# Kernel tuning notes

Measured on AMD Instinct MI355X. Metric: run time of the kernel, lower is better.

## Reference

```python
import jax, jax.numpy as jnp
import numpy as np

N = 100_000      # nodes
E = 1_600_000    # edges (avg degree 16)
IN_DIM = 165
HIDDEN = 64
OUT_DIM = 2


def setup_inputs() -> dict:
    key = jax.random.key(0)
    ks = jax.random.split(key, 10)
    x = jax.random.normal(ks[0], (N, IN_DIM), dtype=jnp.float32)
    edge_index = jax.random.randint(ks[1], (2, E), 0, N, dtype=jnp.int32)
    def lin(k, fan_in, fan_out):
        lim = 1.0 / np.sqrt(fan_in)
        return jax.random.uniform(k, (fan_in, fan_out), jnp.float32, -lim, lim)
    # SAGEConv: lin_l (neighbor path, with bias), lin_r (root path, no bias)
    W1l = lin(ks[2], IN_DIM, HIDDEN); b1 = jnp.zeros((HIDDEN,), jnp.float32)
    W1r = lin(ks[3], IN_DIM, HIDDEN)
    W2l = lin(ks[4], HIDDEN, HIDDEN); b2 = jnp.zeros((HIDDEN,), jnp.float32)
    W2r = lin(ks[5], HIDDEN, HIDDEN)
    Wc = lin(ks[6], HIDDEN, OUT_DIM)
    bc = jax.random.uniform(ks[7], (OUT_DIM,), jnp.float32, -0.1, 0.1)
    return {"x": x, "edge_index": edge_index, "W1l": W1l, "b1": b1, "W1r": W1r,
            "W2l": W2l, "b2": b2, "W2r": W2r, "Wc": Wc, "bc": bc}


def _sage_conv(h, src, dst, Wl, bl, Wr):
    # mean-aggregate source features at destination nodes, then two linears
    msg = h[src]                                              # [E, D] gather
    agg = jax.ops.segment_sum(msg, dst, num_segments=N)       # [N, D] scatter-add
    cnt = jax.ops.segment_sum(jnp.ones((src.shape[0], 1), h.dtype), dst,
                              num_segments=N)                 # [N, 1] in-degree
    mean = agg / jnp.maximum(cnt, 1.0)
    return mean @ Wl + bl + h @ Wr


def reference(x, edge_index, W1l, b1, W1r, W2l, b2, W2r, Wc, bc):
    src, dst = edge_index[0], edge_index[1]
    h = jax.nn.relu(_sage_conv(x, src, dst, W1l, b1, W1r))
    # dropout is a no-op at inference (training=False)
    h = jax.nn.relu(_sage_conv(h, src, dst, W2l, b2, W2r))
    return h @ Wc + bc
```

## Files before the change

kernel.cpp:

```cpp
#include <hip/hip_runtime.h>
#include <hip/hip_fp16.h>
#include <cstdint>

#define NN 100000
#define NE 1600000
#define INDIM 165
#define HID 64
#define KP1 192
#define KP2 64

constexpr int BSH = 7;
constexpr int BNODES = 128;
constexpr int NBUK = (NN + BNODES - 1) / BNODES;
constexpr int SC_CHUNK = 8192;
constexpr int BCAP = 2816;

typedef _Float16 f16x8 __attribute__((ext_vector_type(8)));
typedef _Float16 h2 __attribute__((ext_vector_type(2)));
typedef float f32x4 __attribute__((ext_vector_type(4)));


__global__ __launch_bounds__(256) void k_bscan(const int* __restrict__ bcnt,
                                               int* __restrict__ bbase) {
    __shared__ int wsum[4];
    const int tid = threadIdx.x, lane = tid & 63, wid = tid >> 6;
    int v[4];
    int tsum = 0;
#pragma unroll
    for (int i = 0; i < 4; ++i) {
        int idx = tid * 4 + i;
        v[i] = (idx < NBUK) ? bcnt[idx] : 0;
        tsum += v[i];
    }
    int x = tsum;
#pragma unroll
    for (int off = 1; off < 64; off <<= 1) {
        int y = __shfl_up(x, off, 64);
        if (lane >= off) x += y;
    }
    if (lane == 63) wsum[wid] = x;
    __syncthreads();
    int woff = 0;
#pragma unroll
    for (int w = 0; w < 4; ++w)
        if (w < wid) woff += wsum[w];
    int run = woff + x - tsum;
#pragma unroll
    for (int i = 0; i < 4; ++i) {
        int idx = tid * 4 + i;
        if (idx < NBUK) bbase[idx] = run;
        run += v[i];
    }
    if (tid == 255) bbase[NBUK] = woff + x;
}


__global__ __launch_bounds__(256) void k_scatter(const int* __restrict__ src,
                                                 const int* __restrict__ dst,
                                                 int* __restrict__ bcnt,
                                                 unsigned* __restrict__ Eb, int ne) {
    __shared__ int hist[NBUK];
    __shared__ int base[NBUK];
    const int tid = threadIdx.x;
    const int cs = blockIdx.x * SC_CHUNK;
    for (int b = tid; b < NBUK; b += 256) hist[b] = 0;
    __syncthreads();
    unsigned pack[SC_CHUNK / 256];
#pragma unroll 8
    for (int i = 0; i < SC_CHUNK / 256; ++i) {
        int e = cs + i * 256 + tid;
        if (e < ne) {
            int b = dst[e] >> BSH;
            int r = atomicAdd(&hist[b], 1);
            pack[i] = (unsigned)((b << 13) | r);
        } else {
            pack[i] = 0xFFFFFFFFu;
        }
    }
    __syncthreads();
    for (int b = tid; b < NBUK; b += 256) {
        int c = hist[b];
        base[b] = c ? atomicAdd(&bcnt[b], c) : 0;
    }
    __syncthreads();
#pragma unroll 8
    for (int i = 0; i < SC_CHUNK / 256; ++i) {
        if (pack[i] != 0xFFFFFFFFu) {
            int e = cs + i * 256 + tid;
            int b = pack[i] >> 13, r = pack[i] & 8191;
            int pos = base[b] + r;
            if (pos < BCAP)
                Eb[(size_t)b * BCAP + pos] =
                    (unsigned)src[e] | ((unsigned)(dst[e] & (BNODES - 1)) << 17);
        }
    }
}


__global__ __launch_bounds__(256) void k_csrb(const unsigned* __restrict__ Eb,
                                              const int* __restrict__ bbase,
                                              int* __restrict__ rowptr,
                                              int* __restrict__ col, int n) {
    __shared__ int cnt[BNODES];
    __shared__ int pref[BNODES];
    const int tid = threadIdx.x;
    const int gb = bbase[blockIdx.x];
    const int m = bbase[blockIdx.x + 1] - gb;
    const unsigned* eb = Eb + (size_t)blockIdx.x * BCAP;
    for (int i = tid; i < BNODES; i += 256) cnt[i] = 0;
    __syncthreads();
    for (int e = tid; e < m; e += 256)
        atomicAdd(&cnt[eb[e] >> 17], 1);
    __syncthreads();
    if (tid < 64) {
        int c0 = cnt[tid * 2], c1 = cnt[tid * 2 + 1];
        int s = c0 + c1;
        int x = s;
#pragma unroll
        for (int off = 1; off < 64; off <<= 1) {
            int y = __shfl_up(x, off, 64);
            if (tid >= off) x += y;
        }
        int ex = x - s;
        pref[tid * 2] = ex;
        pref[tid * 2 + 1] = ex + c0;
    }
    __syncthreads();
    const int nodeBase = blockIdx.x * BNODES;
    for (int i = tid; i < BNODES; i += 256) {
        int gn = nodeBase + i;
        if (gn < n) rowptr[gn] = gb + pref[i];
        cnt[i] = 0;
    }
    __syncthreads();
    for (int e = tid; e < m; e += 256) {
        unsigned v = eb[e];
        int d = (int)(v >> 17);
        int r = atomicAdd(&cnt[d], 1);
        col[gb + pref[d] + r] = (int)(v & 0x1FFFFu);
    }
    if (blockIdx.x == 0 && tid == 0) rowptr[n] = bbase[NBUK];
}


__global__ __launch_bounds__(256) void k_cvt(const float* __restrict__ X,
                                             const float* __restrict__ W1l,
                                             const float* __restrict__ W1r,
                                             const float* __restrict__ W2l,
                                             const float* __restrict__ W2r,
                                             _Float16* __restrict__ Xh,
                                             _Float16* __restrict__ Wt1,
                                             _Float16* __restrict__ Wt2) {
    constexpr int XB = (NN * 24) / 256;
    if (blockIdx.x < XB) {
        int g = blockIdx.x * 256 + threadIdx.x;
        int row = g / 24;
        int col0 = (g - row * 24) * 8;
        f16x8 h;
#pragma unroll
        for (int i = 0; i < 8; ++i) {
            int c = col0 + i;
            h[i] = (_Float16)((c < INDIM) ? X[(size_t)row * INDIM + c] : 0.f);
        }
        *(f16x8*)&Xh[(size_t)row * KP1 + col0] = h;
    } else {
        int o = (blockIdx.x - XB) * 256 + threadIdx.x;
        if (o < 128 * KP1) {
            int c = o / KP1, k = o - c * KP1;
            float v = 0.f;
            if (k < INDIM) v = (c < HID) ? W1l[k * HID + c] : W1r[k * HID + (c - HID)];
            Wt1[o] = (_Float16)v;
        } else {
            int p = o - 128 * KP1;
            int c = p / KP2, k = p - c * KP2;
            float v = (c < HID) ? W2l[k * HID + c] : W2r[k * HID + (c - HID)];
            Wt2[p] = (_Float16)v;
        }
    }
}


template <int KPAD>
__global__ __launch_bounds__(256, 4) void k_linear(const _Float16* __restrict__ Xh,
                                                   const _Float16* __restrict__ Wt,
                                                   _Float16* __restrict__ Y,
                                                   _Float16* __restrict__ Rh, int n) {
    const int tid = threadIdx.x;
    const int lane = tid & 63;
    const int w = tid >> 6;
    const int jn = lane & 15;
    const int kq = lane >> 4;
    const int gn0 = blockIdx.x * 64 + w * 16 + jn;
    const int gn = (gn0 < n) ? gn0 : (n - 1);

    const _Float16* xp = Xh + (size_t)gn * KPAD + kq * 8;
    const _Float16* wp = Wt + (size_t)jn * KPAD + kq * 8;

    f16x8 xf[KPAD / 32];
#pragma unroll
    for (int c = 0; c < KPAD / 32; ++c)
        xf[c] = *(const f16x8*)(xp + c * 32);

    f32x4 acc[8];
#pragma unroll
    for (int t = 0; t < 8; ++t) acc[t] = (f32x4){0.f, 0.f, 0.f, 0.f};

#pragma unroll
    for (int c = 0; c < KPAD / 32; ++c) {
#pragma unroll
        for (int t = 0; t < 8; ++t) {
            const f16x8 wa = *(const f16x8*)(wp + t * (16 * KPAD) + c * 32);
            acc[t] = __builtin_amdgcn_mfma_f32_16x16x32_f16(wa, xf[c], acc[t], 0, 0, 0);
        }
    }

    if (gn0 < n) {
#pragma unroll
        for (int t = 0; t < 8; ++t) {
            const int cb = (t & 3) * 16 + kq * 4;
            union { _Float16 h[4]; uint2 u; } u;
#pragma unroll
            for (int r = 0; r < 4; ++r) u.h[r] = (_Float16)acc[t][r];
            _Float16* dstp = (t < 4) ? (Y + (size_t)gn * HID + cb)
                                     : (Rh + (size_t)gn * HID + cb);
            *(uint2*)dstp = u.u;
        }
    }
}


__device__ __forceinline__ void acc2(float& ax, float& ay, h2 v) {
    ax += (float)v[0];
    ay += (float)v[1];
}

template <bool CLS>
__global__ __launch_bounds__(256) void k_agg(const _Float16* __restrict__ Y,
                                             const _Float16* __restrict__ Rm,
                                             const float* __restrict__ bias,
                                             const int* __restrict__ rowptr,
                                             const int* __restrict__ col,
                                             _Float16* __restrict__ H,
                                             const float* __restrict__ Wc,
                                             const float* __restrict__ bc,
                                             float* __restrict__ out, int n) {
    const int lane = threadIdx.x & 63;
    const int node = blockIdx.x * 4 + (threadIdx.x >> 6);
    if (node >= n) return;
    const int half_ = lane >> 5;
    const unsigned fp = (unsigned)(lane & 31);
    const h2* __restrict__ Y2 = (const h2*)Y;
    const int s = rowptr[node], e = rowptr[node + 1];
    float ax0 = 0.f, ay0 = 0.f, ax1 = 0.f, ay1 = 0.f;
    int i = s + half_;
    for (; i + 14 < e; i += 16) {
        int c[8];
#pragma unroll
        for (int j = 0; j < 8; ++j) c[j] = col[i + 2 * j];
        h2 y[8];
#pragma unroll
        for (int j = 0; j < 8; ++j) y[j] = Y2[(unsigned)c[j] * 32u + fp];
#pragma unroll
        for (int j = 0; j < 8; j += 2) {
            acc2(ax0, ay0, y[j]);
            acc2(ax1, ay1, y[j + 1]);
        }
    }
    for (; i + 6 < e; i += 8) {
        int c[4];
#pragma unroll
        for (int j = 0; j < 4; ++j) c[j] = col[i + 2 * j];
        h2 y[4];
#pragma unroll
        for (int j = 0; j < 4; ++j) y[j] = Y2[(unsigned)c[j] * 32u + fp];
        acc2(ax0, ay0, y[0]);
        acc2(ax1, ay1, y[1]);
        acc2(ax0, ay0, y[2]);
        acc2(ax1, ay1, y[3]);
    }
    for (; i < e; i += 2)
        acc2(ax0, ay0, Y2[(unsigned)col[i] * 32u + fp]);
    float ax = ax0 + ax1, ay = ay0 + ay1;
    ax += __shfl_xor(ax, 32, 64);
    ay += __shfl_xor(ay, 32, 64);
    const float vx = __shfl(ax, lane >> 1, 64);
    const float vy = __shfl(ay, lane >> 1, 64);
    const float acc = (lane & 1) ? vy : vx;
    const int deg = e - s;
    float h = acc / (float)(deg > 1 ? deg : 1) + bias[lane] +
              (float)Rm[(size_t)node * HID + lane];
    h = fmaxf(h, 0.f);
    if (!CLS) {
        H[(size_t)node * HID + lane] = (_Float16)h;
    } else {
        float p0 = h * Wc[lane * 2 + 0];
        float p1 = h * Wc[lane * 2 + 1];
#pragma unroll
        for (int off = 32; off > 0; off >>= 1) {
            p0 += __shfl_xor(p0, off, 64);
            p1 += __shfl_xor(p1, off, 64);
        }
        if (lane == 0) {
            out[(size_t)node * 2 + 0] = p0 + bc[0];
            out[(size_t)node * 2 + 1] = p1 + bc[1];
        }
    }
}


extern "C" void kernel_launch(void* const* d_in, const int* in_sizes, int n_in,
                              void* d_out, int out_size, void* d_ws, size_t ws_size,
                              hipStream_t stream) {
    const float* x   = (const float*)d_in[0];
    const int*   ei  = (const int*)d_in[1];
    const float* W1l = (const float*)d_in[2];
    const float* b1  = (const float*)d_in[3];
    const float* W1r = (const float*)d_in[4];
    const float* W2l = (const float*)d_in[5];
    const float* b2  = (const float*)d_in[6];
    const float* W2r = (const float*)d_in[7];
    const float* Wc  = (const float*)d_in[8];
    const float* bc  = (const float*)d_in[9];
    float* out = (float*)d_out;
    const int* src = ei;
    const int* dst = ei + NE;

    char* base = (char*)d_ws;
    size_t off = 0;
    auto alloc = [&](size_t bytes) {
        void* p = base + off;
        off = (off + bytes + 255) & ~(size_t)255;
        return p;
    };
    int*      bcnt    = (int*)alloc((size_t)NBUK * 4);
    int*      bbase   = (int*)alloc((size_t)(NBUK + 1) * 4);
    int*      rowptr  = (int*)alloc((size_t)(NN + 1) * 4);
    int*      col     = (int*)alloc((size_t)NE * 4);
    _Float16* Y       = (_Float16*)alloc((size_t)NN * HID * 2 + 256);
    _Float16* Rh      = (_Float16*)alloc((size_t)NN * HID * 2);
    _Float16* Hh      = (_Float16*)alloc((size_t)NN * HID * 2);
    _Float16* Xh      = (_Float16*)alloc((size_t)NN * KP1 * 2);
    _Float16* Wt1     = (_Float16*)alloc((size_t)128 * KP1 * 2);
    _Float16* Wt2     = (_Float16*)alloc((size_t)128 * KP2 * 2);
    unsigned* Eb      = (unsigned*)Y;

    const int sb = (NE + SC_CHUNK - 1) / SC_CHUNK;
    constexpr int XB = (NN * 24) / 256;
    const int cvb = XB + (128 * KP1 + 128 * KP2 + 255) / 256;

    hipMemsetAsync(bcnt, 0, (size_t)NBUK * 4, stream);
    k_scatter<<<sb, 256, 0, stream>>>(src, dst, bcnt, Eb, NE);
    k_bscan<<<1, 256, 0, stream>>>(bcnt, bbase);
    k_csrb<<<NBUK, 256, 0, stream>>>(Eb, bbase, rowptr, col, NN);

    k_cvt<<<cvb, 256, 0, stream>>>(x, W1l, W1r, W2l, W2r, Xh, Wt1, Wt2);

    k_linear<KP1><<<(NN + 63) / 64, 256, 0, stream>>>(Xh, Wt1, Y, Rh, NN);
    k_agg<false><<<(NN + 3) / 4, 256, 0, stream>>>(Y, Rh, b1, rowptr, col, Hh,
                                                   nullptr, nullptr, nullptr, NN);
    k_linear<KP2><<<(NN + 63) / 64, 256, 0, stream>>>(Hh, Wt2, Y, Rh, NN);
    k_agg<true><<<(NN + 3) / 4, 256, 0, stream>>>(Y, Rh, b2, rowptr, col, nullptr,
                                                  Wc, bc, out, NN);
}
```

Measured before the change: 360.4 us.

## Fuse fp32-to-fp16 input conversion into first linear; widen aggregation gathers to 8 bytes

The first-layer linear kernel now reads the fp32 input features directly and converts them to fp16 in registers, so the separate conversion pass and the padded fp16 copy of X are gone. This drops one full write and read of a roughly 38 MB intermediate. The mean-aggregation kernel now splits each wave into four edge lanes that each gather 4 halves (8 bytes) per load instead of two lanes gathering 2 halves, followed by a wider shuffle reduction. The fused linear makes unaligned scalar fp32 loads, because rows of 165 floats are not vector-aligned, and that may be less efficient than the old pass.

```diff
diff --git a/kernel.cpp b/kernel.cpp
--- a/kernel.cpp
+++ b/kernel.cpp
@@ -16,7 +16,7 @@
 constexpr int BCAP = 2816;
 
 typedef _Float16 f16x8 __attribute__((ext_vector_type(8)));
-typedef _Float16 h2 __attribute__((ext_vector_type(2)));
+typedef _Float16 f16x4 __attribute__((ext_vector_type(4)));
 typedef float f32x4 __attribute__((ext_vector_type(4)));
 
 
@@ -143,38 +143,75 @@
 }
 
 
-__global__ __launch_bounds__(256) void k_cvt(const float* __restrict__ X,
-                                             const float* __restrict__ W1l,
-                                             const float* __restrict__ W1r,
-                                             const float* __restrict__ W2l,
-                                             const float* __restrict__ W2r,
-                                             _Float16* __restrict__ Xh,
-                                             _Float16* __restrict__ Wt1,
-                                             _Float16* __restrict__ Wt2) {
-    constexpr int XB = (NN * 24) / 256;
-    if (blockIdx.x < XB) {
-        int g = blockIdx.x * 256 + threadIdx.x;
-        int row = g / 24;
-        int col0 = (g - row * 24) * 8;
-        f16x8 h;
-#pragma unroll
-        for (int i = 0; i < 8; ++i) {
-            int c = col0 + i;
-            h[i] = (_Float16)((c < INDIM) ? X[(size_t)row * INDIM + c] : 0.f);
-        }
-        *(f16x8*)&Xh[(size_t)row * KP1 + col0] = h;
-    } else {
-        int o = (blockIdx.x - XB) * 256 + threadIdx.x;
-        if (o < 128 * KP1) {
-            int c = o / KP1, k = o - c * KP1;
-            float v = 0.f;
-            if (k < INDIM) v = (c < HID) ? W1l[k * HID + c] : W1r[k * HID + (c - HID)];
-            Wt1[o] = (_Float16)v;
-        } else {
-            int p = o - 128 * KP1;
-            int c = p / KP2, k = p - c * KP2;
-            float v = (c < HID) ? W2l[k * HID + c] : W2r[k * HID + (c - HID)];
-            Wt2[p] = (_Float16)v;
+__global__ __launch_bounds__(256) void k_wcvt(const float* __restrict__ W1l,
+                                              const float* __restrict__ W1r,
+                                              const float* __restrict__ W2l,
+                                              const float* __restrict__ W2r,
+                                              _Float16* __restrict__ Wt1,
+                                              _Float16* __restrict__ Wt2) {
+    int o = blockIdx.x * 256 + threadIdx.x;
+    if (o < 128 * KP1) {
+        int c = o / KP1, k = o - c * KP1;
+        float v = 0.f;
+        if (k < INDIM) v = (c < HID) ? W1l[k * HID + c] : W1r[k * HID + (c - HID)];
+        Wt1[o] = (_Float16)v;
+    } else if (o < 128 * KP1 + 128 * KP2) {
+        int p = o - 128 * KP1;
+        int c = p / KP2, k = p - c * KP2;
+        float v = (c < HID) ? W2l[k * HID + c] : W2r[k * HID + (c - HID)];
+        Wt2[p] = (_Float16)v;
+    }
+}
+
+
+__global__ __launch_bounds__(256, 4) void k_lin1(const float* __restrict__ X,
+                                                 const _Float16* __restrict__ Wt,
+                                                 _Float16* __restrict__ Y,
+                                                 _Float16* __restrict__ Rh, int n) {
+    const int tid = threadIdx.x;
+    const int lane = tid & 63;
+    const int w = tid >> 6;
+    const int jn = lane & 15;
+    const int kq = lane >> 4;
+    const int gn0 = blockIdx.x * 64 + w * 16 + jn;
+    const int gn = (gn0 < n) ? gn0 : (n - 1);
+
+    const float* xp = X + (size_t)gn * INDIM + kq * 8;
+    const _Float16* wp = Wt + (size_t)jn * KP1 + kq * 8;
+
+    f16x8 xf[6];
+#pragma unroll
+    for (int c = 0; c < 5; ++c)
+#pragma unroll
+        for (int j = 0; j < 8; ++j)
+            xf[c][j] = (_Float16)xp[c * 32 + j];
+#pragma unroll
+    for (int j = 0; j < 8; ++j)
+        xf[5][j] = (kq == 0 && j < 5) ? (_Float16)xp[5 * 32 + j] : (_Float16)0.f;
+
+    f32x4 acc[8];
+#pragma unroll
+    for (int t = 0; t < 8; ++t) acc[t] = (f32x4){0.f, 0.f, 0.f, 0.f};
+
+#pragma unroll
+    for (int c = 0; c < 6; ++c) {
+#pragma unroll
+        for (int t = 0; t < 8; ++t) {
+            const f16x8 wa = *(const f16x8*)(wp + t * (16 * KP1) + c * 32);
+            acc[t] = __builtin_amdgcn_mfma_f32_16x16x32_f16(wa, xf[c], acc[t], 0, 0, 0);
+        }
+    }
+
+    if (gn0 < n) {
+#pragma unroll
+        for (int t = 0; t < 8; ++t) {
+            const int cb = (t & 3) * 16 + kq * 4;
+            union { _Float16 h[4]; uint2 u; } u;
+#pragma unroll
+            for (int r = 0; r < 4; ++r) u.h[r] = (_Float16)acc[t][r];
+            _Float16* dstp = (t < 4) ? (Y + (size_t)gn * HID + cb)
+                                     : (Rh + (size_t)gn * HID + cb);
+            *(uint2*)dstp = u.u;
         }
     }
 }
@@ -228,11 +265,6 @@
     }
 }
 
-
-__device__ __forceinline__ void acc2(float& ax, float& ay, h2 v) {
-    ax += (float)v[0];
-    ay += (float)v[1];
-}
 
 template <bool CLS>
 __global__ __launch_bounds__(256) void k_agg(const _Float16* __restrict__ Y,
@@ -247,45 +279,39 @@
     const int lane = threadIdx.x & 63;
     const int node = blockIdx.x * 4 + (threadIdx.x >> 6);
     if (node >= n) return;
-    const int half_ = lane >> 5;
-    const unsigned fp = (unsigned)(lane & 31);
-    const h2* __restrict__ Y2 = (const h2*)Y;
+    const int q = lane >> 4;
+    const unsigned fs = (unsigned)(lane & 15);
+    const f16x4* __restrict__ Y4 = (const f16x4*)Y;
     const int s = rowptr[node], e = rowptr[node + 1];
-    float ax0 = 0.f, ay0 = 0.f, ax1 = 0.f, ay1 = 0.f;
-    int i = s + half_;
-    for (; i + 14 < e; i += 16) {
-        int c[8];
-#pragma unroll
-        for (int j = 0; j < 8; ++j) c[j] = col[i + 2 * j];
-        h2 y[8];
-#pragma unroll
-        for (int j = 0; j < 8; ++j) y[j] = Y2[(unsigned)c[j] * 32u + fp];
-#pragma unroll
-        for (int j = 0; j < 8; j += 2) {
-            acc2(ax0, ay0, y[j]);
-            acc2(ax1, ay1, y[j + 1]);
-        }
-    }
-    for (; i + 6 < e; i += 8) {
-        int c[4];
-#pragma unroll
-        for (int j = 0; j < 4; ++j) c[j] = col[i + 2 * j];
-        h2 y[4];
-#pragma unroll
-        for (int j = 0; j < 4; ++j) y[j] = Y2[(unsigned)c[j] * 32u + fp];
-        acc2(ax0, ay0, y[0]);
-        acc2(ax1, ay1, y[1]);
-        acc2(ax0, ay0, y[2]);
-        acc2(ax1, ay1, y[3]);
-    }
-    for (; i < e; i += 2)
-        acc2(ax0, ay0, Y2[(unsigned)col[i] * 32u + fp]);
-    float ax = ax0 + ax1, ay = ay0 + ay1;
-    ax += __shfl_xor(ax, 32, 64);
-    ay += __shfl_xor(ay, 32, 64);
-    const float vx = __shfl(ax, lane >> 1, 64);
-    const float vy = __shfl(ay, lane >> 1, 64);
-    const float acc = (lane & 1) ? vy : vx;
+    float a0 = 0.f, a1 = 0.f, a2 = 0.f, a3 = 0.f;
+    float b0 = 0.f, b1 = 0.f, b2 = 0.f, b3 = 0.f;
+    int i = s + q;
+    for (; i + 15 < e; i += 16) {
+        int c0 = col[i], c1 = col[i + 4], c2 = col[i + 8], c3 = col[i + 12];
+        f16x4 y0 = Y4[(unsigned)c0 * 16u + fs];
+        f16x4 y1 = Y4[(unsigned)c1 * 16u + fs];
+        f16x4 y2 = Y4[(unsigned)c2 * 16u + fs];
+        f16x4 y3 = Y4[(unsigned)c3 * 16u + fs];
+        a0 += (float)y0[0]; a1 += (float)y0[1]; a2 += (float)y0[2]; a3 += (float)y0[3];
+        b0 += (float)y1[0]; b1 += (float)y1[1]; b2 += (float)y1[2]; b3 += (float)y1[3];
+        a0 += (float)y2[0]; a1 += (float)y2[1]; a2 += (float)y2[2]; a3 += (float)y2[3];
+        b0 += (float)y3[0]; b1 += (float)y3[1]; b2 += (float)y3[2]; b3 += (float)y3[3];
+    }
+    for (; i < e; i += 4) {
+        f16x4 y0 = Y4[(unsigned)col[i] * 16u + fs];
+        a0 += (float)y0[0]; a1 += (float)y0[1]; a2 += (float)y0[2]; a3 += (float)y0[3];
+    }
+    a0 += b0; a1 += b1; a2 += b2; a3 += b3;
+    a0 += __shfl_xor(a0, 16, 64); a0 += __shfl_xor(a0, 32, 64);
+    a1 += __shfl_xor(a1, 16, 64); a1 += __shfl_xor(a1, 32, 64);
+    a2 += __shfl_xor(a2, 16, 64); a2 += __shfl_xor(a2, 32, 64);
+    a3 += __shfl_xor(a3, 16, 64); a3 += __shfl_xor(a3, 32, 64);
+    const float v0 = __shfl(a0, lane >> 2, 64);
+    const float v1 = __shfl(a1, lane >> 2, 64);
+    const float v2 = __shfl(a2, lane >> 2, 64);
+    const float v3 = __shfl(a3, lane >> 2, 64);
+    const int cc = lane & 3;
+    const float acc = (cc == 0) ? v0 : (cc == 1) ? v1 : (cc == 2) ? v2 : v3;
     const int deg = e - s;
     float h = acc / (float)(deg > 1 ? deg : 1) + bias[lane] +
               (float)Rm[(size_t)node * HID + lane];
@@ -339,23 +365,20 @@
     _Float16* Y       = (_Float16*)alloc((size_t)NN * HID * 2 + 256);
     _Float16* Rh      = (_Float16*)alloc((size_t)NN * HID * 2);
     _Float16* Hh      = (_Float16*)alloc((size_t)NN * HID * 2);
-    _Float16* Xh      = (_Float16*)alloc((size_t)NN * KP1 * 2);
     _Float16* Wt1     = (_Float16*)alloc((size_t)128 * KP1 * 2);
     _Float16* Wt2     = (_Float16*)alloc((size_t)128 * KP2 * 2);
     unsigned* Eb      = (unsigned*)Y;
 
     const int sb = (NE + SC_CHUNK - 1) / SC_CHUNK;
-    constexpr int XB = (NN * 24) / 256;
-    const int cvb = XB + (128 * KP1 + 128 * KP2 + 255) / 256;
+    const int wb = (128 * KP1 + 128 * KP2 + 255) / 256;
 
     hipMemsetAsync(bcnt, 0, (size_t)NBUK * 4, stream);
     k_scatter<<<sb, 256, 0, stream>>>(src, dst, bcnt, Eb, NE);
     k_bscan<<<1, 256, 0, stream>>>(bcnt, bbase);
     k_csrb<<<NBUK, 256, 0, stream>>>(Eb, bbase, rowptr, col, NN);
-
-    k_cvt<<<cvb, 256, 0, stream>>>(x, W1l, W1r, W2l, W2r, Xh, Wt1, Wt2);
-
-    k_linear<KP1><<<(NN + 63) / 64, 256, 0, stream>>>(Xh, Wt1, Y, Rh, NN);
+    k_wcvt<<<wb, 256, 0, stream>>>(W1l, W1r, W2l, W2r, Wt1, Wt2);
+
+    k_lin1<<<(NN + 63) / 64, 256, 0, stream>>>(x, Wt1, Y, Rh, NN);
     k_agg<false><<<(NN + 3) / 4, 256, 0, stream>>>(Y, Rh, b1, rowptr, col, Hh,
                                                    nullptr, nullptr, nullptr, NN);
     k_linear<KP2><<<(NN + 63) / 64, 256, 0, stream>>>(Hh, Wt2, Y, Rh, NN);
```

Measured after the change: 339.1 us. 1.06x faster.
